# Kernel tuning notes

Measured on AMD Instinct MI355X. Metric: run time of the kernel, lower is better.

The kernel has to match this reference:

```python
import jax, jax.numpy as jnp
import numpy as np

S = 100        # sos_token_num
H = 12         # num heads
LY = 3         # number of residual blocks
NEG = -100.0   # attention-bias masking value


def layer_norm(x, w, b, eps=1e-5):
    u = jnp.mean(x, -1, keepdims=True)
    v = jnp.mean((x - u) ** 2, -1, keepdims=True)
    return (x - u) / jnp.sqrt(v + eps) * w + b


def quick_gelu(x):
    return x * jax.nn.sigmoid(1.702 * x)


def l2norm(x, eps=1e-12):
    return x / jnp.maximum(jnp.linalg.norm(x, axis=-1, keepdims=True), eps)


def setup_inputs() -> dict:
    key = jax.random.key(0)
    ks = iter(jax.random.split(key, 32))
    n, c, hh, ww, out_dim = 2, 768, 32, 32, 512
    r = lambda shape, s=1.0: jax.random.normal(next(ks), shape, jnp.float32) * s
    return dict(
        cls_token=r((1, n, c)),
        pix_feat=r((n, c, hh, ww)),
        last_surgery=r((1 + hh * ww, n, c)),
        attn_bias=r((n, 1, S, hh, ww)),
        qkv_w=r((LY, 3 * c, c), 0.02), qkv_b=jnp.zeros((LY, 3 * c)),
        proj_w=r((LY, c, c), 0.02), proj_b=jnp.zeros((LY, c)),
        ln1_w=jnp.ones((LY, c)), ln1_b=jnp.zeros((LY, c)),
        ln2_w=jnp.ones((LY, c)), ln2_b=jnp.zeros((LY, c)),
        fc_w=r((LY, 4 * c, c), 0.02), fc_b=jnp.zeros((LY, 4 * c)),
        fc2_w=r((LY, c, 4 * c), 0.02), fc2_b=jnp.zeros((LY, c)),
        lnp_w=jnp.ones((c,)), lnp_b=jnp.zeros((c,)),
        proj_out=r((c, out_dim), 0.02),
    )


def reference(cls_token, pix_feat, last_surgery, attn_bias,
              qkv_w, qkv_b, proj_w, proj_b,
              ln1_w, ln1_b, ln2_w, ln2_b,
              fc_w, fc_b, fc2_w, fc2_b,
              lnp_w, lnp_b, proj_out):
    n, c, hh, ww = pix_feat.shape
    L = hh * ww
    N = S + 1 + L
    d = c // H
    scale = d ** -0.5

    # ---- assemble token streams (batch-first [n, N, c]) ----
    pix_tok = pix_feat.reshape(n, c, L).transpose(2, 0, 1)          # [L, n, c]
    x = jnp.concatenate([jnp.broadcast_to(cls_token, (S, n, c)), cls_token, pix_tok], 0)
    x_sur = jnp.concatenate([jnp.broadcast_to(last_surgery[0:1], (S, n, c)), last_surgery], 0)
    xo = x.transpose(1, 0, 2)      # 'original' stream  [n, N, c]
    xs = x_sur.transpose(1, 0, 2)  # 'surgery'  stream  [n, N, c]

    # ---- build attention biases (identity downsample: bias already at (h, w)) ----
    base = jnp.zeros((N, N), jnp.float32)
    base = base.at[:, :S].set(NEG)
    base = base.at[jnp.arange(S), jnp.arange(S)].set(0.0)
    base = base.at[:S, S].set(NEG)
    plain = jnp.broadcast_to(base, (n, H, N, N))
    bias = jnp.broadcast_to(attn_bias, (n, H, S, hh, ww)).reshape(n, H, S, L)
    biased = plain.at[:, :, :S, S + 1:].set(bias)   # sos rows attend to pixels via bias

    def attention(t, l):
        # t: [n, N, c] (post-ln_1); returns (surgery_res, ori_res)
        qkv = (t @ qkv_w[l].T + qkv_b[l]).reshape(n, N, 3, H, d).transpose(2, 0, 3, 1, 4)
        q, k, v = qkv[0], qkv[1], qkv[2]   # each [n, H, N, d]
        def attend(q_, k_, mask):
            a = jax.nn.softmax(jnp.einsum('bhnd,bhmd->bhnm', q_, k_) * scale + mask, axis=-1)
            o = jnp.einsum('bhnm,bhmd->bhnd', a, v).transpose(0, 2, 1, 3).reshape(n, N, c)
            return o @ proj_w[l].T + proj_b[l]
        x_ori_res = attend(q, k, biased)   # standard pass, biased mask (attn_mask[0])
        x_res = attend(v, v, plain)        # q = k = v surgery pass (attn_mask[1])
        return x_res, x_ori_res

    for l in range(LY):
        t = layer_norm(xo, ln1_w[l], ln1_b[l])
        res_sur, res_ori = attention(t, l)
        xo = xo + res_ori
        xo = xo + (quick_gelu(layer_norm(xo, ln2_w[l], ln2_b[l]) @ fc_w[l].T + fc_b[l]) @ fc2_w[l].T + fc2_b[l])
        xs = xs + res_sur

    # ---- heads ----
    sos = l2norm(layer_norm(xo[:, :S], lnp_w, lnp_b) @ proj_out)          # [n, S, out]
    img = l2norm(layer_norm(xs[:, S:], lnp_w, lnp_b) @ proj_out)          # [n, 1+L, out]
    img = img[:, 1:, :].transpose(0, 2, 1).reshape(n, proj_out.shape[1], hh, ww)
    return sos, img
```

## Files before the change

kernel.cpp:

```cpp
#include <hip/hip_runtime.h>
#include <math.h>


constexpr int Cc = 768;
constexpr int Ss = 100;
constexpr int Hh = 12;
constexpr int Ll = 1024;
constexpr int Nn = 1125;
constexpr int NB = 2;
constexpr int VTS = 1216;
constexpr float QS = 0.18033688011112042f;
constexpr float LOG2E = 1.4426950408889634f;

typedef unsigned short u16;
typedef unsigned int u32;
typedef __attribute__((ext_vector_type(8))) short short8v;
typedef __attribute__((ext_vector_type(8))) unsigned short ushort8v;
typedef __attribute__((ext_vector_type(4))) float f32x4;
typedef __attribute__((ext_vector_type(4))) unsigned int u32x4;

__device__ inline u16 f2bf(float f) {
  unsigned u = __builtin_bit_cast(unsigned int, f);
  unsigned r = u + 0x7fffu + ((u >> 16) & 1u);
  return (u16)(r >> 16);
}
__device__ inline float bf2f(u16 v) {
  return __builtin_bit_cast(float, (unsigned int)v << 16);
}
__device__ inline unsigned cvtpk(float lo, float hi) {
  unsigned r;
  asm("v_cvt_pk_bf16_f32 %0, %1, %2" : "=v"(r) : "v"(lo), "v"(hi));
  return r;
}
__device__ inline float max3f(float a, float b, float c) {
  float r;
  asm("v_max3_f32 %0, %1, %2, %3" : "=v"(r) : "v"(a), "v"(b), "v"(c));
  return r;
}

__device__ inline int swz(int row, int col) {
  return (row << 6) + ((((col >> 3) ^ (row & 7)) << 3) | (col & 7));
}

__global__ __launch_bounds__(256) void assemble_kernel(
    const float* __restrict__ cls, const float* __restrict__ pix,
    const float* __restrict__ sur, float* __restrict__ xo, float* __restrict__ xs) {
  int idx = blockIdx.x * 256 + (int)threadIdx.x;
  int total = NB * Nn * Cc;
  if (idx >= total) return;
  int ch = idx % Cc;
  int t  = (idx / Cc) % Nn;
  int b  = idx / (Cc * Nn);
  float vo, vs;
  if (t <= Ss) vo = cls[b * Cc + ch];
  else         vo = pix[(size_t)b * Cc * Ll + (size_t)ch * Ll + (t - Ss - 1)];
  if (t < Ss)  vs = sur[b * Cc + ch];
  else         vs = sur[(size_t)(t - Ss) * NB * Cc + b * Cc + ch];
  xo[idx] = vo;
  xs[idx] = vs;
}

constexpr int CN0 = 3 * 2304 * 768;
constexpr int CN1 = 3 * 768 * 768;
constexpr int CN2 = 3 * 3072 * 768;
constexpr int CN3 = 3 * 768 * 3072;
__global__ __launch_bounds__(256) void cvt4_kernel(
    const float* __restrict__ s0, const float* __restrict__ s1,
    const float* __restrict__ s2, const float* __restrict__ s3,
    u16* __restrict__ dst) {
  int i4 = (blockIdx.x * 256 + (int)threadIdx.x) * 4;
  if (i4 >= CN0 + CN1 + CN2 + CN3) return;
  const float* src; int off;
  if (i4 < CN0)             { src = s0; off = i4; }
  else if (i4 < CN0 + CN1)  { src = s1; off = i4 - CN0; }
  else if (i4 < CN0 + CN1 + CN2) { src = s2; off = i4 - CN0 - CN1; }
  else                      { src = s3; off = i4 - CN0 - CN1 - CN2; }
  float4 v = *(const float4*)(src + off);
  *(ushort4*)(dst + i4) = make_ushort4(f2bf(v.x), f2bf(v.y), f2bf(v.z), f2bf(v.w));
}

__global__ __launch_bounds__(256) void transpose_po_kernel(
    const float* __restrict__ in, u16* __restrict__ out) {
  int id = blockIdx.x * 256 + (int)threadIdx.x;
  if (id >= 512 * 768) return;
  int nidx = id / 768, k = id - nidx * 768;
  out[id] = f2bf(in[(size_t)k * 512 + nidx]);
}

__global__ __launch_bounds__(256) void vtrans_kernel(
    const u16* __restrict__ qkv, u16* __restrict__ vtg) {
  __shared__ u16 tile[64][72];
  int tt = blockIdx.x;
  int bh = blockIdx.y;
  int b = bh / Hh, h = bh - b * Hh;
  int tid = (int)threadIdx.x;
  {
    int tl = tid >> 2, c0 = (tid & 3) << 4;
    int tok = tt * 64 + tl;
    int tokc = tok > 1124 ? 1124 : tok;
    const u16* src = qkv + ((size_t)(b * Nn + tokc)) * 2304 + 2 * Cc + h * 64 + c0;
    ushort8v v0 = *(const ushort8v*)src;
    ushort8v v1 = *(const ushort8v*)(src + 8);
    if (tok > 1124) { v0 = (ushort8v)0; v1 = (ushort8v)0; }
    *(ushort8v*)&tile[tl][c0] = v0;
    *(ushort8v*)&tile[tl][c0 + 8] = v1;
  }
  __syncthreads();
  {
    int d = tid >> 2, t0 = (tid & 3) << 4;
    ushort8v o0, o1;
#pragma unroll
    for (int j = 0; j < 8; ++j) { o0[j] = tile[t0 + j][d]; o1[j] = tile[t0 + 8 + j][d]; }
    size_t orow = ((size_t)bh * 64 + d) * VTS + tt * 64 + t0;
    *(ushort8v*)&vtg[orow] = o0;
    *(ushort8v*)&vtg[orow + 8] = o1;
  }
}

__global__ __launch_bounds__(256) void ln_kernel(
    const float* __restrict__ X, const float* __restrict__ w, const float* __restrict__ b,
    u16* __restrict__ Y, int rows_per_b, int row_off) {
  int r = blockIdx.x;
  int bb = r / rows_per_b;
  int i  = r % rows_per_b;
  const float* x = X + ((size_t)bb * Nn + row_off + i) * Cc;
  u16* y = Y + (size_t)r * Cc;
  int tid = (int)threadIdx.x;
  float v0 = x[tid], v1 = x[tid + 256], v2 = x[tid + 512];
  float s = v0 + v1 + v2;
  __shared__ float sbuf[4];
  for (int off = 32; off; off >>= 1) s += __shfl_xor(s, off);
  if ((tid & 63) == 0) sbuf[tid >> 6] = s;
  __syncthreads();
  float mean = (sbuf[0] + sbuf[1] + sbuf[2] + sbuf[3]) * (1.0f / Cc);
  float d0 = v0 - mean, d1 = v1 - mean, d2 = v2 - mean;
  float q = d0 * d0 + d1 * d1 + d2 * d2;
  __syncthreads();
  for (int off = 32; off; off >>= 1) q += __shfl_xor(q, off);
  if ((tid & 63) == 0) sbuf[tid >> 6] = q;
  __syncthreads();
  float var = (sbuf[0] + sbuf[1] + sbuf[2] + sbuf[3]) * (1.0f / Cc);
  float inv = rsqrtf(var + 1e-5f);
  y[tid]       = f2bf(d0 * inv * w[tid]       + b[tid]);
  y[tid + 256] = f2bf(d1 * inv * w[tid + 256] + b[tid + 256]);
  y[tid + 512] = f2bf(d2 * inv * w[tid + 512] + b[tid + 512]);
}

__global__ __launch_bounds__(256) void gemm128_kernel(
    const u16* __restrict__ A, const u16* __restrict__ B,
    const float* __restrict__ bias, u16* __restrict__ outb,
    int M, int N, int K, int act) {
  __shared__ __align__(16) u16 Als[128 * 64];
  __shared__ __align__(16) u16 Bls[128 * 64];
  int tid = (int)threadIdx.x;
  int wave = tid >> 6, lane = tid & 63, g = lane >> 4, li = lane & 15;
  int wm = wave >> 1, wn = wave & 1;
  int row0 = blockIdx.y * 128, col0 = blockIdx.x * 128;

  const u16* aptr[4]; const u16* bptr[4]; int dsti[4];
#pragma unroll
  for (int j = 0; j < 4; ++j) {
    int c = tid + j * 256;
    int r = c >> 3, c8 = c & 7;
    dsti[j] = (r << 6) + ((c8 ^ (r & 7)) << 3);
    int ra = row0 + r; if (ra > M - 1) ra = M - 1;
    aptr[j] = A + (size_t)ra * K + (c8 << 3);
    bptr[j] = B + (size_t)(col0 + r) * K + (c8 << 3);
  }

  f32x4 acc[4][4];
#pragma unroll
  for (int mi = 0; mi < 4; ++mi)
#pragma unroll
    for (int ni = 0; ni < 4; ++ni) acc[mi][ni] = (f32x4){0.f, 0.f, 0.f, 0.f};

  for (int k0 = 0; k0 < K; k0 += 64) {
    ushort8v ta[4], tb[4];
#pragma unroll
    for (int j = 0; j < 4; ++j) {
      ta[j] = *(const ushort8v*)(aptr[j] + k0);
      tb[j] = *(const ushort8v*)(bptr[j] + k0);
    }
    __syncthreads();
#pragma unroll
    for (int j = 0; j < 4; ++j) {
      *(ushort8v*)&Als[dsti[j]] = ta[j];
      *(ushort8v*)&Bls[dsti[j]] = tb[j];
    }
    __syncthreads();
#pragma unroll
    for (int kc = 0; kc < 2; ++kc) {
      short8v af[4], bfr[4];
#pragma unroll
      for (int mi = 0; mi < 4; ++mi) {
        int rr = wm * 64 + mi * 16 + li;
        af[mi] = *(const short8v*)&Als[(rr << 6) + (((kc * 4 + g) ^ (rr & 7)) << 3)];
      }
#pragma unroll
      for (int ni = 0; ni < 4; ++ni) {
        int rb = wn * 64 + ni * 16 + li;
        bfr[ni] = *(const short8v*)&Bls[(rb << 6) + (((kc * 4 + g) ^ (rb & 7)) << 3)];
      }
      __builtin_amdgcn_s_setprio(1);
#pragma unroll
      for (int mi = 0; mi < 4; ++mi)
#pragma unroll
        for (int ni = 0; ni < 4; ++ni)
          acc[mi][ni] = __builtin_amdgcn_mfma_f32_16x16x32_bf16(af[mi], bfr[ni], acc[mi][ni], 0, 0, 0);
      __builtin_amdgcn_s_setprio(0);
    }
  }

#pragma unroll
  for (int mi = 0; mi < 4; ++mi) {
#pragma unroll
    for (int r = 0; r < 4; ++r) {
      int m = row0 + wm * 64 + mi * 16 + g * 4 + r;
      if (m >= M) continue;
#pragma unroll
      for (int ni = 0; ni < 4; ++ni) {
        int n = col0 + wn * 64 + ni * 16 + li;
        float v = acc[mi][ni][r];
        if (bias) v += bias[n];
        if (act)  v = v / (1.0f + __expf(-1.702f * v));
        outb[(size_t)m * N + n] = f2bf(v);
      }
    }
  }
}

__global__ __launch_bounds__(256) void gemm64_kernel(
    const u16* __restrict__ A0, const u16* __restrict__ A1,
    const u16* __restrict__ B, const float* __restrict__ bias,
    const float* __restrict__ res0, const float* __restrict__ res1,
    float* __restrict__ outf0, float* __restrict__ outf1,
    u16* __restrict__ outb0, u16* __restrict__ outb1,
    int M, int N, int K, int act) {
  __shared__ __align__(16) u16 Als[64 * 64];
  __shared__ __align__(16) u16 Bls[128 * 64];
  int zz = blockIdx.z;
  const u16* A = zz ? A1 : A0;
  const float* res = zz ? res1 : res0;
  float* outf = zz ? outf1 : outf0;
  u16* outb = zz ? outb1 : outb0;
  int tid = (int)threadIdx.x;
  int wave = tid >> 6, lane = tid & 63, g = lane >> 4, li = lane & 15;
  int row0 = blockIdx.y * 64, col0 = blockIdx.x * 128;

  const u16* aptr[2]; int dA[2];
#pragma unroll
  for (int j = 0; j < 2; ++j) {
    int ca = tid + j * 256;
    int r = ca >> 3, c8 = ca & 7;
    dA[j] = (r << 6) + ((c8 ^ (r & 7)) << 3);
    int ra = row0 + r; if (ra > M - 1) ra = M - 1;
    aptr[j] = A + (size_t)ra * K + (c8 << 3);
  }
  const u16* bptr[4]; int dB[4];
#pragma unroll
  for (int j = 0; j < 4; ++j) {
    int cb = tid + j * 256;
    int r = cb >> 3, c8 = cb & 7;
    dB[j] = (r << 6) + ((c8 ^ (r & 7)) << 3);
    bptr[j] = B + (size_t)(col0 + r) * K + (c8 << 3);
  }

  f32x4 acc[4][2];
#pragma unroll
  for (int mi = 0; mi < 4; ++mi)
#pragma unroll
    for (int ni = 0; ni < 2; ++ni) acc[mi][ni] = (f32x4){0.f, 0.f, 0.f, 0.f};

  for (int k0 = 0; k0 < K; k0 += 64) {
    ushort8v ta[2], tb[4];
#pragma unroll
    for (int j = 0; j < 2; ++j) ta[j] = *(const ushort8v*)(aptr[j] + k0);
#pragma unroll
    for (int j = 0; j < 4; ++j) tb[j] = *(const ushort8v*)(bptr[j] + k0);
    __syncthreads();
#pragma unroll
    for (int j = 0; j < 2; ++j) *(ushort8v*)&Als[dA[j]] = ta[j];
#pragma unroll
    for (int j = 0; j < 4; ++j) *(ushort8v*)&Bls[dB[j]] = tb[j];
    __syncthreads();
#pragma unroll
    for (int kc = 0; kc < 2; ++kc) {
      short8v af[4], bfr[2];
#pragma unroll
      for (int mi = 0; mi < 4; ++mi) {
        int rr = mi * 16 + li;
        af[mi] = *(const short8v*)&Als[(rr << 6) + (((kc * 4 + g) ^ (rr & 7)) << 3)];
      }
#pragma unroll
      for (int ni = 0; ni < 2; ++ni) {
        int rb = wave * 32 + ni * 16 + li;
        bfr[ni] = *(const short8v*)&Bls[(rb << 6) + (((kc * 4 + g) ^ (rb & 7)) << 3)];
      }
      __builtin_amdgcn_s_setprio(1);
#pragma unroll
      for (int mi = 0; mi < 4; ++mi)
#pragma unroll
        for (int ni = 0; ni < 2; ++ni)
          acc[mi][ni] = __builtin_amdgcn_mfma_f32_16x16x32_bf16(af[mi], bfr[ni], acc[mi][ni], 0, 0, 0);
      __builtin_amdgcn_s_setprio(0);
    }
  }

#pragma unroll
  for (int mi = 0; mi < 4; ++mi) {
#pragma unroll
    for (int r = 0; r < 4; ++r) {
      int m = row0 + mi * 16 + g * 4 + r;
      if (m >= M) continue;
#pragma unroll
      for (int ni = 0; ni < 2; ++ni) {
        int n = col0 + wave * 32 + ni * 16 + li;
        float v = acc[mi][ni][r];
        if (bias) v += bias[n];
        if (act)  v = v / (1.0f + __expf(-1.702f * v));
        if (res)  v += res[(size_t)m * N + n];
        if (outf) outf[(size_t)m * N + n] = v;
        else      outb[(size_t)m * N + n] = f2bf(v);
      }
    }
  }
}

__global__ __launch_bounds__(256) void attn_kernel(
    const u16* __restrict__ qkv, const u16* __restrict__ vtg,
    const float* __restrict__ abias,
    u16* __restrict__ ao, u16* __restrict__ as_) {
  __shared__ __align__(16) u16 Klds[64 * 64];
  __shared__ __align__(16) u16 Vt[64 * 64];
  int id = (int)blockIdx.x;
  int virt = (id & 7) * 114 + (id >> 3);
  int gid = virt / 19;
  int qt  = virt - gid * 19;
  int z   = gid / 24;
  int bh  = gid - z * 24;
  int b = bh / Hh, h = bh - b * Hh;
  int tid = (int)threadIdx.x;
  int wave = tid >> 6, lane = tid & 63, g = lane >> 4, li = lane & 15;
  bool sosq = qt >= 17;
  u16* outp = z ? as_ : ao;

  int qbase = sosq ? (qt - 17) * 64 + wave * 16 : Ss + qt * 64 + wave * 16;
  int qtok = qbase + li;
  int qcap = sosq ? 99 : 1124;
  if (qtok > qcap) qtok = qcap;
  int qoff = z ? 2 * Cc + h * 64 : h * 64;
  int koff = z ? 2 * Cc + h * 64 : Cc + h * 64;

  short8v qf[2];
  {
    const u16* qp = qkv + ((size_t)b * Nn + qtok) * 2304 + qoff;
#pragma unroll
    for (int kc = 0; kc < 2; ++kc) {
      ushort8v a = *(const ushort8v*)(qp + kc * 32 + g * 8);
      u32x4 w;
#pragma unroll
      for (int jj = 0; jj < 4; ++jj)
        w[jj] = cvtpk(bf2f(a[2 * jj]) * QS, bf2f(a[2 * jj + 1]) * QS);
      qf[kc] = __builtin_bit_cast(short8v, w);
    }
  }

  int skey = tid >> 2;
  int sd0  = (tid & 3) << 4;
  int prow = 16 * (2 * (skey >> 5) + ((skey >> 2) & 1)) + 4 * ((skey >> 3) & 3) + (skey & 3);
  int kK0 = swz(prow, sd0), kK1 = swz(prow, sd0 + 8);
  int vI0 = swz(skey, sd0), vI1 = swz(skey, sd0 + 8);
  const u16* kbase = qkv + (size_t)b * Nn * 2304 + koff + sd0;
  const u16* vbase = vtg + ((size_t)bh * 64 + skey) * VTS + sd0;

  const int KOFF[4] = {0, 4, 32, 36};

  f32x4 oacc[4];
#pragma unroll
  for (int dt = 0; dt < 4; ++dt) oacc[dt] = (f32x4){0.f, 0.f, 0.f, 0.f};
  float mrow = -1e30f, lrow = 0.f;

  int NT = sosq ? 18 : 17;
  for (int kt = 0; kt < NT; ++kt) {
    int t0 = sosq ? (kt == 0 ? (qt - 17) * 64 : 64 * kt + 32) : 96 + 64 * kt;
    __syncthreads();
    {
      int ktok = t0 + skey; if (ktok > 1124) ktok = 1124;
      const u16* kp = kbase + (size_t)ktok * 2304;
      ushort8v k0v = *(const ushort8v*)kp;
      ushort8v k1v = *(const ushort8v*)(kp + 8);
      const u16* vp = vbase + t0;
      ushort8v v0 = *(const ushort8v*)vp;
      ushort8v v1 = *(const ushort8v*)(vp + 8);
      *(ushort8v*)&Klds[kK0] = k0v;
      *(ushort8v*)&Klds[kK1] = k1v;
      *(ushort8v*)&Vt[vI0] = v0;
      *(ushort8v*)&Vt[vI1] = v1;
    }
    __syncthreads();

    f32x4 sacc[4];
#pragma unroll
    for (int nt = 0; nt < 4; ++nt) sacc[nt] = (f32x4){0.f, 0.f, 0.f, 0.f};
    __builtin_amdgcn_s_setprio(1);
#pragma unroll
    for (int kc = 0; kc < 2; ++kc) {
#pragma unroll
      for (int nt = 0; nt < 4; ++nt) {
        short8v kb = *(const short8v*)&Klds[swz(nt * 16 + li, kc * 32 + g * 8)];
        sacc[nt] = __builtin_amdgcn_mfma_f32_16x16x32_bf16(kb, qf[kc], sacc[nt], 0, 0, 0);
      }
    }
    __builtin_amdgcn_s_setprio(0);

    int tg = t0 + 8 * g;
    if (!sosq) {
      if (kt == 0) {
#pragma unroll
        for (int nt = 0; nt < 4; ++nt)
#pragma unroll
          for (int r = 0; r < 4; ++r)
            if (tg + KOFF[nt] + r < 100) sacc[nt][r] = -1e30f;
      } else if (kt == 16) {
#pragma unroll
        for (int nt = 0; nt < 4; ++nt)
#pragma unroll
          for (int r = 0; r < 4; ++r)
            if (tg + KOFF[nt] + r > 1124) sacc[nt][r] = -1e30f;
      }
    } else {
      if (kt == 0) {
#pragma unroll
        for (int nt = 0; nt < 4; ++nt)
#pragma unroll
          for (int r = 0; r < 4; ++r)
            if (tg + KOFF[nt] + r != qtok) sacc[nt][r] = -1e30f;
      } else if (z == 0) {
        const float* bp = abias + ((size_t)b * Ss + qtok) * Ll;
#pragma unroll
        for (int nt = 0; nt < 4; ++nt)
#pragma unroll
          for (int r = 0; r < 4; ++r) {
            int tok = tg + KOFF[nt] + r;
            int bi = tok - 101; bi = bi < 0 ? 0 : bi; bi = bi > 1023 ? 1023 : bi;
            float bv = bp[bi];
            bool bad = (tok < 101) | (tok > 1124);
            sacc[nt][r] = bad ? -1e30f : fmaf(bv, LOG2E, sacc[nt][r]);
          }
      } else {
#pragma unroll
        for (int nt = 0; nt < 4; ++nt)
#pragma unroll
          for (int r = 0; r < 4; ++r) {
            int tok = tg + KOFF[nt] + r;
            if ((tok < 101) | (tok > 1124)) sacc[nt][r] = -1e30f;
          }
      }
    }

    float rmax = max3f(sacc[0][0], sacc[0][1], sacc[0][2]);
    rmax = max3f(rmax, sacc[0][3], sacc[1][0]);
    rmax = max3f(rmax, sacc[1][1], sacc[1][2]);
    rmax = max3f(rmax, sacc[1][3], sacc[2][0]);
    rmax = max3f(rmax, sacc[2][1], sacc[2][2]);
    rmax = max3f(rmax, sacc[2][3], sacc[3][0]);
    rmax = max3f(rmax, sacc[3][1], sacc[3][2]);
    rmax = fmaxf(rmax, sacc[3][3]);
    rmax = fmaxf(rmax, __shfl_xor(rmax, 16));
    rmax = fmaxf(rmax, __shfl_xor(rmax, 32));
    float mnew = fmaxf(mrow, rmax);
    float fac = __builtin_amdgcn_exp2f(mrow - mnew);
    mrow = mnew;
    float psum = 0.f;
#pragma unroll
    for (int nt = 0; nt < 4; ++nt)
#pragma unroll
      for (int r = 0; r < 4; ++r) {
        float e = __builtin_amdgcn_exp2f(sacc[nt][r] - mnew);
        sacc[nt][r] = e;
        psum += e;
      }
    psum += __shfl_xor(psum, 16);
    psum += __shfl_xor(psum, 32);
    lrow = lrow * fac + psum;
#pragma unroll
    for (int dt = 0; dt < 4; ++dt) oacc[dt] *= fac;

    __builtin_amdgcn_s_setprio(1);
#pragma unroll
    for (int kcp = 0; kcp < 2; ++kcp) {
      u32x4 pwv;
#pragma unroll
      for (int w = 0; w < 4; ++w) {
        int nt = 2 * kcp + (w >> 1);
        int r0 = (w & 1) * 2;
        pwv[w] = cvtpk(sacc[nt][r0], sacc[nt][r0 + 1]);
      }
      short8v pb = __builtin_bit_cast(short8v, pwv);
#pragma unroll
      for (int dt = 0; dt < 4; ++dt) {
        short8v va = *(const short8v*)&Vt[swz(dt * 16 + li, kcp * 32 + g * 8)];
        oacc[dt] = __builtin_amdgcn_mfma_f32_16x16x32_bf16(va, pb, oacc[dt], 0, 0, 0);
      }
    }
    __builtin_amdgcn_s_setprio(0);
  }

  int tok = qbase + li;
  if (tok <= qcap) {
    float inv = 1.0f / lrow;
    u16* op = outp + ((size_t)b * Nn + tok) * Cc + h * 64 + g * 4;
#pragma unroll
    for (int dt = 0; dt < 4; ++dt) {
      unsigned lo = cvtpk(oacc[dt][0] * inv, oacc[dt][1] * inv);
      unsigned hi = cvtpk(oacc[dt][2] * inv, oacc[dt][3] * inv);
      uint2 o2; o2.x = lo; o2.y = hi;
      *(uint2*)(op + dt * 16) = o2;
    }
  }
}

__global__ __launch_bounds__(256) void l2norm_sos_kernel(
    const float* __restrict__ Xp, float* __restrict__ out) {
  int r = blockIdx.x;
  int tid = (int)threadIdx.x;
  const float* x = Xp + (size_t)r * 512;
  float v0 = x[tid], v1 = x[tid + 256];
  float s = v0 * v0 + v1 * v1;
  __shared__ float sbuf[4];
  for (int off = 32; off; off >>= 1) s += __shfl_xor(s, off);
  if ((tid & 63) == 0) sbuf[tid >> 6] = s;
  __syncthreads();
  float tot = sbuf[0] + sbuf[1] + sbuf[2] + sbuf[3];
  float inv = 1.0f / fmaxf(sqrtf(tot), 1e-12f);
  out[(size_t)r * 512 + tid]       = v0 * inv;
  out[(size_t)r * 512 + tid + 256] = v1 * inv;
}

__global__ __launch_bounds__(256) void l2norm_img_kernel(
    const float* __restrict__ Xp, float* __restrict__ out) {
  int r = blockIdx.x;
  int b = r / 1025, ti = r % 1025;
  int tid = (int)threadIdx.x;
  const float* x = Xp + (size_t)r * 512;
  float v0 = x[tid], v1 = x[tid + 256];
  float s = v0 * v0 + v1 * v1;
  __shared__ float sbuf[4];
  for (int off = 32; off; off >>= 1) s += __shfl_xor(s, off);
  if ((tid & 63) == 0) sbuf[tid >> 6] = s;
  __syncthreads();
  float tot = sbuf[0] + sbuf[1] + sbuf[2] + sbuf[3];
  if (ti == 0) return;
  float inv = 1.0f / fmaxf(sqrtf(tot), 1e-12f);
  float* o = out + (size_t)b * 512 * 1024 + (ti - 1);
  o[(size_t)tid * 1024]         = v0 * inv;
  o[(size_t)(tid + 256) * 1024] = v1 * inv;
}

extern "C" void kernel_launch(void* const* d_in, const int* in_sizes, int n_in,
                              void* d_out, int out_size, void* d_ws, size_t ws_size,
                              hipStream_t stream) {
  const float* cls      = (const float*)d_in[0];
  const float* pix      = (const float*)d_in[1];
  const float* sur      = (const float*)d_in[2];
  const float* abias    = (const float*)d_in[3];
  const float* qkv_w    = (const float*)d_in[4];
  const float* qkv_b    = (const float*)d_in[5];
  const float* proj_w   = (const float*)d_in[6];
  const float* proj_b   = (const float*)d_in[7];
  const float* ln1_w    = (const float*)d_in[8];
  const float* ln1_b    = (const float*)d_in[9];
  const float* ln2_w    = (const float*)d_in[10];
  const float* ln2_b    = (const float*)d_in[11];
  const float* fc_w     = (const float*)d_in[12];
  const float* fc_b     = (const float*)d_in[13];
  const float* fc2_w    = (const float*)d_in[14];
  const float* fc2_b    = (const float*)d_in[15];
  const float* lnp_w    = (const float*)d_in[16];
  const float* lnp_b    = (const float*)d_in[17];
  const float* proj_o   = (const float*)d_in[18];
  float* out = (float*)d_out;

  const size_t SZ = (size_t)NB * Nn * Cc;
  float* xo      = (float*)d_ws;
  float* xs      = xo + SZ;
  float* head_pj = xs + SZ;
  u16* tln_bf = (u16*)(head_pj + 2250 * 512);
  u16* act_bf = tln_bf + (size_t)2250 * 768;
  u16* ao_bf  = act_bf + (size_t)2250 * 3072;
  u16* as_bf  = ao_bf + (size_t)2250 * 768;
  u16* wq_bf  = as_bf + (size_t)2250 * 768;
  u16* wp_bf  = wq_bf + (size_t)CN0;
  u16* wf_bf  = wp_bf + (size_t)CN1;
  u16* w2_bf  = wf_bf + (size_t)CN2;
  u16* wo_bf  = w2_bf + (size_t)CN3;
  u16* vtg    = wo_bf + (size_t)512 * 768;

  assemble_kernel<<<6750, 256, 0, stream>>>(cls, pix, sur, xo, xs);
  cvt4_kernel<<<20736, 256, 0, stream>>>(qkv_w, proj_w, fc_w, fc2_w, wq_bf);
  transpose_po_kernel<<<1536, 256, 0, stream>>>(proj_o, wo_bf);

  for (int l = 0; l < 3; ++l) {
    ln_kernel<<<2250, 256, 0, stream>>>(xo, ln1_w + l * 768, ln1_b + l * 768, tln_bf, Nn, 0);
    gemm128_kernel<<<dim3(18, 18), 256, 0, stream>>>(
        tln_bf, wq_bf + (size_t)l * 2304 * 768, qkv_b + l * 2304,
        act_bf, 2250, 2304, 768, 0);
    vtrans_kernel<<<dim3(19, 24), 256, 0, stream>>>(act_bf, vtg);
    attn_kernel<<<912, 256, 0, stream>>>(act_bf, vtg, abias, ao_bf, as_bf);
    gemm64_kernel<<<dim3(6, 36, 2), 256, 0, stream>>>(
        ao_bf, as_bf, wp_bf + (size_t)l * 768 * 768, proj_b + l * 768,
        xo, xs, xo, xs, nullptr, nullptr, 2250, 768, 768, 0);
    ln_kernel<<<2250, 256, 0, stream>>>(xo, ln2_w + l * 768, ln2_b + l * 768, tln_bf, Nn, 0);
    gemm128_kernel<<<dim3(24, 18), 256, 0, stream>>>(
        tln_bf, wf_bf + (size_t)l * 3072 * 768, fc_b + l * 3072,
        act_bf, 2250, 3072, 768, 1);
    gemm64_kernel<<<dim3(6, 36, 1), 256, 0, stream>>>(
        act_bf, act_bf, w2_bf + (size_t)l * 768 * 3072, fc2_b + l * 768,
        xo, xo, xo, xo, nullptr, nullptr, 2250, 768, 3072, 0);
  }

  ln_kernel<<<200, 256, 0, stream>>>(xo, lnp_w, lnp_b, tln_bf, 100, 0);
  ln_kernel<<<2050, 256, 0, stream>>>(xs, lnp_w, lnp_b, tln_bf + 200 * 768, 1025, 100);
  gemm64_kernel<<<dim3(4, 36, 1), 256, 0, stream>>>(
      tln_bf, tln_bf, wo_bf, nullptr,
      nullptr, nullptr, head_pj, head_pj, nullptr, nullptr, 2250, 512, 768, 0);
  l2norm_sos_kernel<<<200, 256, 0, stream>>>(head_pj, out);
  l2norm_img_kernel<<<2050, 256, 0, stream>>>(head_pj + 200 * 512, out + 102400);
}
```

Baseline: 775.0 us.

## Split attention KV range in two halves with a separate combine kernel

```diff
diff --git a/kernel.cpp b/kernel.cpp
--- a/kernel.cpp
+++ b/kernel.cpp
@@ -329,20 +329,21 @@
 __global__ __launch_bounds__(256) void attn_kernel(
     const u16* __restrict__ qkv, const u16* __restrict__ vtg,
     const float* __restrict__ abias,
-    u16* __restrict__ ao, u16* __restrict__ as_) {
+    float* __restrict__ opart, float* __restrict__ mlp) {
   __shared__ __align__(16) u16 Klds[64 * 64];
   __shared__ __align__(16) u16 Vt[64 * 64];
   int id = (int)blockIdx.x;
-  int virt = (id & 7) * 114 + (id >> 3);
-  int gid = virt / 19;
-  int qt  = virt - gid * 19;
-  int z   = gid / 24;
-  int bh  = gid - z * 24;
+  int virt = (id & 7) * 228 + (id >> 3);
+  int gidh = virt / 19;
+  int qt   = virt - gidh * 19;
+  int half = gidh & 1;
+  int gid  = gidh >> 1;
+  int z    = gid / 24;
+  int bh   = gid - z * 24;
   int b = bh / Hh, h = bh - b * Hh;
   int tid = (int)threadIdx.x;
   int wave = tid >> 6, lane = tid & 63, g = lane >> 4, li = lane & 15;
   bool sosq = qt >= 17;
-  u16* outp = z ? as_ : ao;
 
   int qbase = sosq ? (qt - 17) * 64 + wave * 16 : Ss + qt * 64 + wave * 16;
   int qtok = qbase + li;
@@ -381,7 +382,9 @@
   float mrow = -1e30f, lrow = 0.f;
 
   int NT = sosq ? 18 : 17;
-  for (int kt = 0; kt < NT; ++kt) {
+  int kt0 = half * 9;
+  int kt1 = half ? NT : 9;
+  for (int kt = kt0; kt < kt1; ++kt) {
     int t0 = sosq ? (kt == 0 ? (qt - 17) * 64 : 64 * kt + 32) : 96 + 64 * kt;
     __syncthreads();
     {
@@ -508,15 +511,44 @@
 
   int tok = qbase + li;
   if (tok <= qcap) {
-    float inv = 1.0f / lrow;
-    u16* op = outp + ((size_t)b * Nn + tok) * Cc + h * 64 + g * 4;
-#pragma unroll
-    for (int dt = 0; dt < 4; ++dt) {
-      unsigned lo = cvtpk(oacc[dt][0] * inv, oacc[dt][1] * inv);
-      unsigned hi = cvtpk(oacc[dt][2] * inv, oacc[dt][3] * inv);
-      uint2 o2; o2.x = lo; o2.y = hi;
-      *(uint2*)(op + dt * 16) = o2;
-    }
+    int hp = half * 2 + z;
+    float* op = opart + ((size_t)hp * NB * Nn + (size_t)b * Nn + tok) * Cc + h * 64 + g * 4;
+#pragma unroll
+    for (int dt = 0; dt < 4; ++dt)
+      *(float4*)(op + dt * 16) = make_float4(oacc[dt][0], oacc[dt][1], oacc[dt][2], oacc[dt][3]);
+    if (g == 0) {
+      size_t mb = (((size_t)hp * 24 + bh) * Nn + tok) * 2;
+      mlp[mb] = mrow;
+      mlp[mb + 1] = lrow;
+    }
+  }
+}
+
+__global__ __launch_bounds__(256) void attn_combine_kernel(
+    const float* __restrict__ opart, const float* __restrict__ mlp,
+    u16* __restrict__ ao, u16* __restrict__ as_) {
+  int blk = blockIdx.x;
+  int pass = blk / (NB * Nn);
+  int row = blk - pass * (NB * Nn);
+  int b = row / Nn, i = row - b * Nn;
+  u16* outp = pass ? as_ : ao;
+  int tid = (int)threadIdx.x;
+#pragma unroll
+  for (int e = 0; e < 3; ++e) {
+    int c = tid + e * 256;
+    int h = c >> 6;
+    int bh = b * Hh + h;
+    size_t m0i = (((size_t)(0 * 2 + pass) * 24 + bh) * Nn + i) * 2;
+    size_t m1i = (((size_t)(1 * 2 + pass) * 24 + bh) * Nn + i) * 2;
+    float m0 = mlp[m0i], l0 = mlp[m0i + 1];
+    float m1 = mlp[m1i], l1 = mlp[m1i + 1];
+    float M = fmaxf(m0, m1);
+    float w0 = __builtin_amdgcn_exp2f(m0 - M);
+    float w1 = __builtin_amdgcn_exp2f(m1 - M);
+    float L = l0 * w0 + l1 * w1;
+    float v0 = opart[((size_t)(0 * 2 + pass) * NB * Nn + row) * Cc + c];
+    float v1 = opart[((size_t)(1 * 2 + pass) * NB * Nn + row) * Cc + c];
+    outp[(size_t)row * Cc + c] = f2bf((v0 * w0 + v1 * w1) / L);
   }
 }
 
@@ -582,10 +614,12 @@
   float* out = (float*)d_out;
 
   const size_t SZ = (size_t)NB * Nn * Cc;
-  float* xo      = (float*)d_ws;
-  float* xs      = xo + SZ;
-  float* head_pj = xs + SZ;
-  u16* tln_bf = (u16*)(head_pj + 2250 * 512);
+  float* xo    = (float*)d_ws;
+  float* xs    = xo + SZ;
+  float* opart = xs + SZ;
+  float* mlp   = opart + (size_t)4 * 2250 * 768;
+  float* head_pj = opart;
+  u16* tln_bf = (u16*)(mlp + (size_t)4 * 24 * 1125 * 2);
   u16* act_bf = tln_bf + (size_t)2250 * 768;
   u16* ao_bf  = act_bf + (size_t)2250 * 3072;
   u16* as_bf  = ao_bf + (size_t)2250 * 768;
@@ -606,7 +640,8 @@
         tln_bf, wq_bf + (size_t)l * 2304 * 768, qkv_b + l * 2304,
         act_bf, 2250, 2304, 768, 0);
     vtrans_kernel<<<dim3(19, 24), 256, 0, stream>>>(act_bf, vtg);
-    attn_kernel<<<912, 256, 0, stream>>>(act_bf, vtg, abias, ao_bf, as_bf);
+    attn_kernel<<<1824, 256, 0, stream>>>(act_bf, vtg, abias, opart, mlp);
+    attn_combine_kernel<<<4500, 256, 0, stream>>>(opart, mlp, ao_bf, as_bf);
     gemm64_kernel<<<dim3(6, 36, 2), 256, 0, stream>>>(
         ao_bf, as_bf, wp_bf + (size_t)l * 768 * 768, proj_b + l * 768,
         xo, xs, xo, xs, nullptr, nullptr, 2250, 768, 768, 0);
```

Result: faster. 753.5 us (median of 2 runs) (-2.8%).
